# Optimization experiments

Measured on AMD Instinct MI355X. Metric: run time of the kernel, lower is better.

Reference implementation:

```python
import jax, jax.numpy as jnp
import numpy as np

B, N, F_IN, H, H4, F_OUT = 4096, 256, 15, 128, 32, 6


def setup_inputs() -> dict:
    key = jax.random.key(0)
    ks = jax.random.split(key, 12)
    inp = {
        "x_feat": jax.random.normal(ks[0], (B, N, F_IN), dtype=jnp.float32),
        "coords": jax.random.normal(ks[1], (B, N, 3), dtype=jnp.float32),
        "mask": jnp.ones((B, N, 1), dtype=jnp.float32),
        "centers": jax.random.randint(ks[2], (B,), 0, N),
        # node_mlp: Linear(15,H) SiLU Linear(H,H) SiLU
        "nW1": jax.random.normal(ks[3], (F_IN, H), dtype=jnp.float32) / np.sqrt(F_IN),
        "nb1": jnp.zeros((H,), jnp.float32),
        "nW2": jax.random.normal(ks[4], (H, H), dtype=jnp.float32) / np.sqrt(H),
        "nb2": jnp.zeros((H,), jnp.float32),
        # edge_mlp: Linear(1,H//4) SiLU Linear(H//4,1) Sigmoid
        "eW1": jax.random.normal(ks[5], (1, H4), dtype=jnp.float32),
        "eb1": jnp.zeros((H4,), jnp.float32),
        "eW2": jax.random.normal(ks[6], (H4, 1), dtype=jnp.float32) / np.sqrt(H4),
        "eb2": jnp.zeros((1,), jnp.float32),
        # readout: Linear(H,H) SiLU Linear(H,6)
        "rW1": jax.random.normal(ks[7], (H, H), dtype=jnp.float32) / np.sqrt(H),
        "rb1": jnp.zeros((H,), jnp.float32),
        "rW2": jax.random.normal(ks[8], (H, F_OUT), dtype=jnp.float32) / np.sqrt(H),
        "rb2": jnp.zeros((F_OUT,), jnp.float32),
    }
    return inp


def reference(x_feat, coords, mask, centers,
              nW1, nb1, nW2, nb2,
              eW1, eb1, eW2, eb2,
              rW1, rb1, rW2, rb2):
    silu = jax.nn.silu
    # node MLP: (B,N,15) -> (B,N,H), masked
    h = silu(silu(x_feat @ nW1 + nb1) @ nW2 + nb2) * mask
    # gather center coords: (B,3)
    c_idx = centers[:, None, None]
    c0 = jnp.take_along_axis(coords, jnp.broadcast_to(c_idx, (coords.shape[0], 1, 3)), axis=1)[:, 0]
    # distances to center: (B,N,1)
    d = jnp.linalg.norm(coords - c0[:, None, :], axis=-1, keepdims=True)
    # edge MLP on scalar distance -> sigmoid weight, masked
    w = jax.nn.sigmoid(silu(d @ eW1 + eb1) @ eW2 + eb2) * mask
    # gather center hidden state: (B,H)
    h_center = jnp.take_along_axis(h, jnp.broadcast_to(c_idx, (h.shape[0], 1, h.shape[2])), axis=1)[:, 0]
    # weighted message sum to center node
    msg_sum = (w * h).sum(axis=1) + h_center  # (B,H)
    # readout: (B,6)
    return silu(msg_sum @ rW1 + rb1) @ rW2 + rb2
```

## Files before the change

kernel.cpp:

```cpp
#include <hip/hip_runtime.h>
#include <math.h>

#define BB 4096
#define NN 256
#define FIN 15
#define HH 128
#define HH4 32
#define FOUT 6

typedef __attribute__((ext_vector_type(8))) short short8v;
typedef __attribute__((ext_vector_type(4))) float f32x4;
typedef __attribute__((ext_vector_type(2))) float f32x2;

__device__ __forceinline__ float exp_raw(float x) {
    float r;
    asm("v_exp_f32 %0, %1" : "=v"(r) : "v"(x));
    return r;
}

__device__ __forceinline__ float silu_f(float z) {
    return z * __builtin_amdgcn_rcpf(1.0f + __expf(-z));
}
__device__ __forceinline__ float sigm_f(float z) {
    return __builtin_amdgcn_rcpf(1.0f + __expf(-z));
}

__device__ __forceinline__ f32x2 silu2(float a, float b) {
    const f32x2 z = {a, b};
    const f32x2 zs = z * (f32x2){-1.44269504088896340736f, -1.44269504088896340736f};
    f32x2 e;
    e.x = exp_raw(zs.x);
    e.y = exp_raw(zs.y);
    const f32x2 den = e + (f32x2){1.0f, 1.0f};
    f32x2 r;
    r.x = __builtin_amdgcn_rcpf(den.x);
    r.y = __builtin_amdgcn_rcpf(den.y);
    return z * r;
}

__device__ __forceinline__ unsigned short f2bf(float f) {
    unsigned int u = __builtin_bit_cast(unsigned int, f);
    u += 0x7FFFu + ((u >> 16) & 1u);
    return (unsigned short)(u >> 16);
}

__device__ __forceinline__ unsigned int cvt_pk_bf16(float lo, float hi) {
    unsigned int r;
    asm("v_cvt_pk_bf16_f32 %0, %1, %2" : "=v"(r) : "v"(lo), "v"(hi));
    return r;
}

__global__ void prep_kernel(const float* __restrict__ nW1,
                            const float* __restrict__ nW2,
                            const float* __restrict__ eW1,
                            const float* __restrict__ eb1,
                            const float* __restrict__ eW2,
                            const float* __restrict__ eb2,
                            unsigned short* __restrict__ ws) {
    const int idx = blockIdx.x * 256 + threadIdx.x;
    if (idx < 4096) {
        const int n = idx >> 5, k = idx & 31;
        ws[idx] = (k < FIN) ? f2bf(nW1[k * HH + n]) : (unsigned short)0;
    } else if (idx < 20480) {
        const int j = idx - 4096;
        const int n = j >> 7, kp = j & 127;
        const int k = 32 * (kp >> 5) + 16 * (kp & 1) + ((kp & 31) >> 1);
        ws[idx] = f2bf(nW2[k * HH + n]);
    } else if (idx < 20480 + 2052) {
        const int i = idx - 20480;
        const float d = (float)i * (1.0f / 128.0f);
        float s = eb2[0];
        #pragma unroll
        for (int t = 0; t < HH4; ++t) {
            float z = d * eW1[t] + eb1[t];
            s += silu_f(z) * eW2[t];
        }
        float* etab = (float*)(ws + 20480);
        etab[i] = sigm_f(s);
    }
}

#define MFMA16(A, B, C) __builtin_amdgcn_mfma_f32_16x16x32_bf16((A), (B), (C), 0, 0, 0)

__launch_bounds__(256)
__global__ void stargnn_kernel(
    const float* __restrict__ x_feat,
    const float* __restrict__ coords,
    const float* __restrict__ mask,
    const int*   __restrict__ centers,
    const float* __restrict__ nb1, const float* __restrict__ nb2,
    const float* __restrict__ rW1, const float* __restrict__ rb1,
    const float* __restrict__ rW2, const float* __restrict__ rb2,
    const unsigned short* __restrict__ wbf,
    float* __restrict__ out)
{
    const int b   = blockIdx.x;
    const int tid = threadIdx.x;
    const int wv  = tid >> 6;
    const int l   = tid & 63;
    const int lr  = l & 15;
    const int lg  = l >> 4;

    const int col0 = wv * 32 + lr;
    const int col1 = wv * 32 + 16 + lr;

    __shared__ __align__(16) unsigned int xbf[64 * 8];
    __shared__ __align__(16) unsigned int h1dw[64 * 64];
    __shared__ __align__(16) float wns[NN];

    const int c = centers[b];

    {
        const float* cb = coords + (size_t)b * NN * 3;
        const float c0x = cb[c*3+0], c0y = cb[c*3+1], c0z = cb[c*3+2];
        const float dx = cb[tid*3+0] - c0x;
        const float dy = cb[tid*3+1] - c0y;
        const float dz = cb[tid*3+2] - c0z;
        const float d  = sqrtf(dx*dx + dy*dy + dz*dz);
        const float* etab = (const float*)(wbf + 20480);
        float t = d * 128.0f;
        t = fminf(t, 2047.0f);
        const int   i  = (int)t;
        const float fr = t - (float)i;
        const float v0 = etab[i];
        const float v1 = etab[i + 1];
        const float w  = v0 + fr * (v1 - v0);
        const float m  = mask[(size_t)b * NN + tid];
        wns[tid] = w * m * m + ((tid == c) ? m : 0.0f);
    }

    const float nb1c0 = nb1[col0], nb1c1 = nb1[col1];
    const float nb2c0 = nb2[col0], nb2c1 = nb2[col1];
    const f32x4 b1i0 = {nb1c0, nb1c0, nb1c0, nb1c0};
    const f32x4 b1i1 = {nb1c1, nb1c1, nb1c1, nb1c1};
    const f32x4 b2i0 = {nb2c0, nb2c0, nb2c0, nb2c0};
    const f32x4 b2i1 = {nb2c1, nb2c1, nb2c1, nb2c1};

    const short8v* w1tp = (const short8v*)wbf;
    const short8v* w2tp = (const short8v*)(wbf + 4096);
    const short8v b1f0 = w1tp[col0 * 4 + lg];
    const short8v b1f1 = w1tp[col1 * 4 + lg];
    const short8v b2f00 = w2tp[col0 * 16 + 0  + lg];
    const short8v b2f01 = w2tp[col0 * 16 + 4  + lg];
    const short8v b2f02 = w2tp[col0 * 16 + 8  + lg];
    const short8v b2f03 = w2tp[col0 * 16 + 12 + lg];
    const short8v b2f10 = w2tp[col1 * 16 + 0  + lg];
    const short8v b2f11 = w2tp[col1 * 16 + 4  + lg];
    const short8v b2f12 = w2tp[col1 * 16 + 8  + lg];
    const short8v b2f13 = w2tp[col1 * 16 + 12 + lg];

    f32x2 maccs = {0.f, 0.f};
    const short8v azero = {0,0,0,0,0,0,0,0};

    const int snode = tid >> 2;
    const int skq   = tid & 3;
    const float* xbase = x_feat + ((size_t)b * NN + snode) * FIN + skq * 4;
    float f0, f1, f2, f3;
    {
        const float* xr = xbase;
        f0 = xr[0]; f1 = xr[1]; f2 = xr[2];
        f3 = (skq < 3) ? xr[3] : 0.0f;
    }

    const int wgrp = (16 * wv + lr) >> 2;
    const int wsub = lr & 3;

    for (int q = 0; q < 4; ++q) {
        xbf[snode * 8 + skq * 2 + 0] = cvt_pk_bf16(f0, f1);
        xbf[snode * 8 + skq * 2 + 1] = cvt_pk_bf16(f2, f3);
        __syncthreads();

        if (q < 3) {
            const float* xr = xbase + (q + 1) * 64 * FIN;
            f0 = xr[0]; f1 = xr[1]; f2 = xr[2];
            f3 = (skq < 3) ? xr[3] : 0.0f;
        }

        #pragma unroll 1
        for (int mt = 0; mt < 4; ++mt) {
            short8v a = azero;
            if (lg < 2)
                a = *(const short8v*)&xbf[(mt * 16 + lr) * 8 + lg * 4];
            f32x4 d0 = MFMA16(a, b1f0, b1i0);
            f32x4 d1 = MFMA16(a, b1f1, b1i1);
            #define H1W(r) { \
                const int row = mt * 16 + lg * 4 + (r); \
                const int gs  = wgrp ^ (lg * 4 + (r)); \
                const f32x2 s = silu2(d0[r], d1[r]); \
                h1dw[row * 64 + gs * 4 + wsub] = cvt_pk_bf16(s.x, s.y); }
            H1W(0) H1W(1) H1W(2) H1W(3)
            #undef H1W
        }
        __syncthreads();

        #pragma unroll 1
        for (int mt = 0; mt < 4; ++mt) {
            const unsigned int* rbase = h1dw + (mt * 16 + lr) * 64;
            const short8v a0 = *(const short8v*)(rbase + (((0  + lg) ^ lr) << 2));
            const short8v a1 = *(const short8v*)(rbase + (((4  + lg) ^ lr) << 2));
            const short8v a2 = *(const short8v*)(rbase + (((8  + lg) ^ lr) << 2));
            const short8v a3 = *(const short8v*)(rbase + (((12 + lg) ^ lr) << 2));
            f32x4 acc0 = b2i0, acc1 = b2i1;
            acc0 = MFMA16(a0, b2f00, acc0);
            acc0 = MFMA16(a1, b2f01, acc0);
            acc0 = MFMA16(a2, b2f02, acc0);
            acc0 = MFMA16(a3, b2f03, acc0);
            acc1 = MFMA16(a0, b2f10, acc1);
            acc1 = MFMA16(a1, b2f11, acc1);
            acc1 = MFMA16(a2, b2f12, acc1);
            acc1 = MFMA16(a3, b2f13, acc1);

            const f32x4 mw4 = *(const f32x4*)&wns[q * 64 + mt * 16 + lg * 4];
            #define EPIR(r) { \
                const f32x2 s = silu2(acc0[r], acc1[r]); \
                const f32x2 mw2 = {mw4[r], mw4[r]}; \
                maccs += mw2 * s; }
            EPIR(0) EPIR(1) EPIR(2) EPIR(3)
            #undef EPIR
        }
    }

    float* msgs  = (float*)h1dw;
    float* part2 = (float*)h1dw + 128;
    float* r1s   = (float*)h1dw + 384;

    float macc0 = maccs.x, macc1 = maccs.y;
    macc0 += __shfl_xor(macc0, 16);
    macc0 += __shfl_xor(macc0, 32);
    macc1 += __shfl_xor(macc1, 16);
    macc1 += __shfl_xor(macc1, 32);
    __syncthreads();
    if (lg == 0) {
        msgs[col0] = macc0;
        msgs[col1] = macc1;
    }
    __syncthreads();

    {
        const int j  = tid & 127;
        const int kh = tid >> 7;
        float acc = 0.f;
        #pragma unroll 8
        for (int k = kh * 64; k < kh * 64 + 64; ++k)
            acc += msgs[k] * rW1[k * HH + j];
        part2[kh * HH + j] = acc;
    }
    __syncthreads();
    if (tid < HH)
        r1s[tid] = silu_f(part2[tid] + part2[HH + tid] + rb1[tid]);
    __syncthreads();

    if (tid < 32 * FOUT) {
        const int j  = tid >> 5;
        const int kk = tid & 31;
        float acc = 0.f;
        #pragma unroll
        for (int q2 = 0; q2 < 4; ++q2) {
            const int k = kk * 4 + q2;
            acc += r1s[k] * rW2[k * FOUT + j];
        }
        acc += __shfl_xor(acc, 1);
        acc += __shfl_xor(acc, 2);
        acc += __shfl_xor(acc, 4);
        acc += __shfl_xor(acc, 8);
        acc += __shfl_xor(acc, 16);
        if (kk == 0) out[(size_t)b * FOUT + j] = acc + rb2[j];
    }
}

extern "C" void kernel_launch(void* const* d_in, const int* in_sizes, int n_in,
                              void* d_out, int out_size, void* d_ws, size_t ws_size,
                              hipStream_t stream) {
    const float* x_feat = (const float*)d_in[0];
    const float* coords = (const float*)d_in[1];
    const float* mask   = (const float*)d_in[2];
    const int*   ctr    = (const int*)d_in[3];
    const float* nW1 = (const float*)d_in[4];
    const float* nb1 = (const float*)d_in[5];
    const float* nW2 = (const float*)d_in[6];
    const float* nb2 = (const float*)d_in[7];
    const float* eW1 = (const float*)d_in[8];
    const float* eb1 = (const float*)d_in[9];
    const float* eW2 = (const float*)d_in[10];
    const float* eb2 = (const float*)d_in[11];
    const float* rW1 = (const float*)d_in[12];
    const float* rb1 = (const float*)d_in[13];
    const float* rW2 = (const float*)d_in[14];
    const float* rb2 = (const float*)d_in[15];
    float* out = (float*)d_out;
    unsigned short* wbf = (unsigned short*)d_ws;

    prep_kernel<<<dim3(89), dim3(256), 0, stream>>>(nW1, nW2, eW1, eb1, eW2, eb2, wbf);
    stargnn_kernel<<<dim3(BB), dim3(256), 0, stream>>>(
        x_feat, coords, mask, ctr,
        nb1, nb2, rW1, rb1, rW2, rb2, wbf, out);
}
```

Baseline: 100.3 us.

## Double block to 512 threads, splitting node rows across two wave halves

Each graph is now processed by 512 threads (8 waves): waves are grouped into two row-halves, each handling 64 of 128 nodes per iteration, so the node loop runs 2 iterations instead of 4. Per-half message partials are reduced through shared memory, and the readout matvec is split four ways over K. This aims to raise per-block parallelism and cut serial loop steps, at the cost of doubled LDS usage, larger blocks, extra barriers and possibly lower occupancy from register pressure under the 512 launch bound.

```diff
diff --git a/kernel.cpp b/kernel.cpp
--- a/kernel.cpp
+++ b/kernel.cpp
@@ -82,7 +82,7 @@
 
 #define MFMA16(A, B, C) __builtin_amdgcn_mfma_f32_16x16x32_bf16((A), (B), (C), 0, 0, 0)
 
-__launch_bounds__(256)
+__launch_bounds__(512)
 __global__ void stargnn_kernel(
     const float* __restrict__ x_feat,
     const float* __restrict__ coords,
@@ -97,20 +97,22 @@
     const int b   = blockIdx.x;
     const int tid = threadIdx.x;
     const int wv  = tid >> 6;
+    const int wvc = wv & 3;
+    const int rh  = wv >> 2;
     const int l   = tid & 63;
     const int lr  = l & 15;
     const int lg  = l >> 4;
 
-    const int col0 = wv * 32 + lr;
-    const int col1 = wv * 32 + 16 + lr;
-
-    __shared__ __align__(16) unsigned int xbf[64 * 8];
-    __shared__ __align__(16) unsigned int h1dw[64 * 64];
+    const int col0 = wvc * 32 + lr;
+    const int col1 = wvc * 32 + 16 + lr;
+
+    __shared__ __align__(16) unsigned int xbf[128 * 8];
+    __shared__ __align__(16) unsigned int h1dw[128 * 64];
     __shared__ __align__(16) float wns[NN];
 
     const int c = centers[b];
 
-    {
+    if (tid < NN) {
         const float* cb = coords + (size_t)b * NN * 3;
         const float c0x = cb[c*3+0], c0y = cb[c*3+1], c0z = cb[c*3+2];
         const float dx = cb[tid*3+0] - c0x;
@@ -162,22 +164,23 @@
         f3 = (skq < 3) ? xr[3] : 0.0f;
     }
 
-    const int wgrp = (16 * wv + lr) >> 2;
+    const int wgrp = (16 * wvc + lr) >> 2;
     const int wsub = lr & 3;
 
-    for (int q = 0; q < 4; ++q) {
+    for (int q = 0; q < 2; ++q) {
         xbf[snode * 8 + skq * 2 + 0] = cvt_pk_bf16(f0, f1);
         xbf[snode * 8 + skq * 2 + 1] = cvt_pk_bf16(f2, f3);
         __syncthreads();
 
-        if (q < 3) {
-            const float* xr = xbase + (q + 1) * 64 * FIN;
+        if (q < 1) {
+            const float* xr = xbase + 128 * FIN;
             f0 = xr[0]; f1 = xr[1]; f2 = xr[2];
             f3 = (skq < 3) ? xr[3] : 0.0f;
         }
 
         #pragma unroll 1
-        for (int mt = 0; mt < 4; ++mt) {
+        for (int mi = 0; mi < 4; ++mi) {
+            const int mt = rh * 4 + mi;
             short8v a = azero;
             if (lg < 2)
                 a = *(const short8v*)&xbf[(mt * 16 + lr) * 8 + lg * 4];
@@ -194,7 +197,8 @@
         __syncthreads();
 
         #pragma unroll 1
-        for (int mt = 0; mt < 4; ++mt) {
+        for (int mi = 0; mi < 4; ++mi) {
+            const int mt = rh * 4 + mi;
             const unsigned int* rbase = h1dw + (mt * 16 + lr) * 64;
             const short8v a0 = *(const short8v*)(rbase + (((0  + lg) ^ lr) << 2));
             const short8v a1 = *(const short8v*)(rbase + (((4  + lg) ^ lr) << 2));
@@ -210,7 +214,7 @@
             acc1 = MFMA16(a2, b2f12, acc1);
             acc1 = MFMA16(a3, b2f13, acc1);
 
-            const f32x4 mw4 = *(const f32x4*)&wns[q * 64 + mt * 16 + lg * 4];
+            const f32x4 mw4 = *(const f32x4*)&wns[q * 128 + mt * 16 + lg * 4];
             #define EPIR(r) { \
                 const f32x2 s = silu2(acc0[r], acc1[r]); \
                 const f32x2 mw2 = {mw4[r], mw4[r]}; \
@@ -222,7 +226,8 @@
 
     float* msgs  = (float*)h1dw;
     float* part2 = (float*)h1dw + 128;
-    float* r1s   = (float*)h1dw + 384;
+    float* part4 = (float*)h1dw + 384;
+    float* r1s   = (float*)h1dw + 896;
 
     float macc0 = maccs.x, macc1 = maccs.y;
     macc0 += __shfl_xor(macc0, 16);
@@ -231,23 +236,26 @@
     macc1 += __shfl_xor(macc1, 32);
     __syncthreads();
     if (lg == 0) {
-        msgs[col0] = macc0;
-        msgs[col1] = macc1;
-    }
+        part2[rh * HH + col0] = macc0;
+        part2[rh * HH + col1] = macc1;
+    }
+    __syncthreads();
+    if (tid < HH) msgs[tid] = part2[tid] + part2[HH + tid];
     __syncthreads();
 
     {
         const int j  = tid & 127;
-        const int kh = tid >> 7;
+        const int kq = tid >> 7;
         float acc = 0.f;
         #pragma unroll 8
-        for (int k = kh * 64; k < kh * 64 + 64; ++k)
+        for (int k = kq * 32; k < kq * 32 + 32; ++k)
             acc += msgs[k] * rW1[k * HH + j];
-        part2[kh * HH + j] = acc;
+        part4[kq * HH + j] = acc;
     }
     __syncthreads();
     if (tid < HH)
-        r1s[tid] = silu_f(part2[tid] + part2[HH + tid] + rb1[tid]);
+        r1s[tid] = silu_f(part4[tid] + part4[HH + tid] + part4[2 * HH + tid]
+                          + part4[3 * HH + tid] + rb1[tid]);
     __syncthreads();
 
     if (tid < 32 * FOUT) {
@@ -291,7 +299,7 @@
     unsigned short* wbf = (unsigned short*)d_ws;
 
     prep_kernel<<<dim3(89), dim3(256), 0, stream>>>(nW1, nW2, eW1, eb1, eW2, eb2, wbf);
-    stargnn_kernel<<<dim3(BB), dim3(256), 0, stream>>>(
+    stargnn_kernel<<<dim3(BB), dim3(512), 0, stream>>>(
         x_feat, coords, mask, ctr,
         nb1, nb2, rW1, rb1, rW2, rb2, wbf, out);
 }
```

After: 108.6 us. 1.08x slower.
